# Performance work log

Measured on AMD Instinct MI355X. Metric: run time of the kernel, lower is better.

Reference implementation:

```python
import jax, jax.numpy as jnp
import numpy as np

N_NODES = 40000
N_EDGES = 640000
IN_DIM = 128
HID_DIM = 128


def _glorot(key, shape):
    fan_in, fan_out = shape[1], shape[0]
    lim = np.sqrt(6.0 / (fan_in + fan_out))
    return jax.random.uniform(key, shape, jnp.float32, -lim, lim)


def setup_inputs() -> dict:
    key = jax.random.key(0)
    ks = jax.random.split(key, 8)
    x = jax.random.normal(ks[0], (N_NODES, IN_DIM), dtype=jnp.float32)
    edge_index = jax.random.randint(ks[1], (2, N_EDGES), 0, N_NODES, dtype=jnp.int64)
    # SAGEConv params: lin_l (applied to aggregated neighbors, has bias), lin_r (self, no bias)
    W1l = _glorot(ks[2], (HID_DIM, IN_DIM))
    b1l = jnp.zeros((HID_DIM,), jnp.float32)
    W1r = _glorot(ks[3], (HID_DIM, IN_DIM))
    W2l = _glorot(ks[4], (HID_DIM, HID_DIM))
    b2l = jnp.zeros((HID_DIM,), jnp.float32)
    W2r = _glorot(ks[5], (HID_DIM, HID_DIM))
    return {"x": x, "edge_index": edge_index, "W1l": W1l, "b1l": b1l,
            "W1r": W1r, "W2l": W2l, "b2l": b2l, "W2r": W2r}


def _sage_conv(x, src, dst, Wl, bl, Wr):
    # mean aggregation of source features into destination nodes
    msg = x[src]  # [E, D] gather
    agg = jax.ops.segment_sum(msg, dst, num_segments=N_NODES)          # [N, D]
    cnt = jax.ops.segment_sum(jnp.ones_like(dst, jnp.float32), dst,
                              num_segments=N_NODES)                     # [N]
    mean = agg / jnp.maximum(cnt, 1.0)[:, None]
    # out = lin_l(mean_neighbors) + lin_r(x)
    return mean @ Wl.T + bl + x @ Wr.T


def reference(x, edge_index, W1l, b1l, W1r, W2l, b2l, W2r):
    src, dst = edge_index[0], edge_index[1]
    h = jax.nn.relu(_sage_conv(x, src, dst, W1l, b1l, W1r))
    h = jax.nn.relu(_sage_conv(h, src, dst, W2l, b2l, W2r))
    return h
```

## Files before the change

### kernel.cpp

```cpp
#include <hip/hip_runtime.h>
#include <hip/hip_bf16.h>

#define DIM 128
#define NN 40000
#define NE 640000
#define NBLK ((NN + 255) / 256)

typedef __attribute__((ext_vector_type(8))) short s16x8;
typedef __attribute__((ext_vector_type(4))) float f32x4;
typedef __attribute__((ext_vector_type(4))) unsigned short u16x4;
typedef __attribute__((ext_vector_type(4))) unsigned int u32x4;

__device__ __forceinline__ float bf16_lo(unsigned v) { return __uint_as_float(v << 16); }
__device__ __forceinline__ float bf16_hi(unsigned v) { return __uint_as_float(v & 0xffff0000u); }
__device__ __forceinline__ unsigned short f_to_bf16(float f) {
    unsigned u = __float_as_uint(f);
    u += 0x7fffu + ((u >> 16) & 1u);
    return (unsigned short)(u >> 16);
}

__global__ void fill_const_f32(float* __restrict__ out, int n, float v) {
    int i = blockIdx.x * blockDim.x + threadIdx.x;
    if (i < n) out[i] = v;
}

__global__ void cvt_all(const float* __restrict__ x, unsigned short* __restrict__ xb,
                        const float* __restrict__ w0, const float* __restrict__ w1,
                        const float* __restrict__ w2, const float* __restrict__ w3,
                        unsigned short* __restrict__ wb) {
    int b = blockIdx.x;
    const float* src;
    unsigned short* dst;
    size_t i;
    if (b < 5000) {
        src = x; dst = xb;
        i = (size_t)b * 256 + threadIdx.x;
    } else {
        int w = b - 5000;
        int m = w >> 4;
        src = (m == 0) ? w0 : (m == 1) ? w1 : (m == 2) ? w2 : w3;
        dst = wb + (size_t)m * 16384;
        i = (size_t)(w & 15) * 256 + threadIdx.x;
    }
    f32x4 v = *(const f32x4*)(src + 4 * i);
    u16x4 o;
    o.x = f_to_bf16(v.x); o.y = f_to_bf16(v.y);
    o.z = f_to_bf16(v.z); o.w = f_to_bf16(v.w);
    *(u16x4*)(dst + 4 * i) = o;
}

__global__ void zero_detect(int* __restrict__ deg, const int* __restrict__ ei,
                            int* __restrict__ flag) {
    int i = blockIdx.x * blockDim.x + threadIdx.x;
    if (i < NN) deg[i] = 0;
    if (blockIdx.x == 0 && threadIdx.x < 64) {
        int w = ei[2 * threadIdx.x + 1];
        unsigned long long m = __ballot(w == 0);
        if (threadIdx.x == 0) *flag = (m == ~0ull) ? 1 : 0;
    }
}


__global__ void count_deg(const int* __restrict__ ei, const int* __restrict__ fmt,
                          int* __restrict__ deg) {
    int e = blockIdx.x * blockDim.x + threadIdx.x;
    if (e >= NE) return;
    int dst = (*fmt) ? ((const int2*)ei)[NE + e].x : ei[NE + e];
    if ((unsigned)dst < (unsigned)NN) atomicAdd(&deg[dst], 1);
}

__global__ void block_sums(const int* __restrict__ deg, int* __restrict__ bsum) {
    __shared__ int sh[256];
    int i = blockIdx.x * 256 + threadIdx.x;
    sh[threadIdx.x] = (i < NN) ? deg[i] : 0;
    __syncthreads();
    for (int off = 128; off > 0; off >>= 1) {
        if (threadIdx.x < off) sh[threadIdx.x] += sh[threadIdx.x + off];
        __syncthreads();
    }
    if (threadIdx.x == 0) bsum[blockIdx.x] = sh[0];
}

__global__ void scan_bsums(int* __restrict__ bsum, int nb) {
    __shared__ int sh[256];
    int t = threadIdx.x;
    int v = (t < nb) ? bsum[t] : 0;
    sh[t] = v;
    __syncthreads();
    for (int off = 1; off < 256; off <<= 1) {
        int u = (t >= off) ? sh[t - off] : 0;
        __syncthreads();
        sh[t] += u;
        __syncthreads();
    }
    if (t < nb) bsum[t] = sh[t] - v;
}

__global__ void scan_block(const int* __restrict__ deg, const int* __restrict__ bsum,
                           int* __restrict__ row_ptr, int* __restrict__ cursor) {
    __shared__ int sh[256];
    int t = threadIdx.x;
    int i = blockIdx.x * 256 + t;
    int v = (i < NN) ? deg[i] : 0;
    sh[t] = v;
    __syncthreads();
    for (int off = 1; off < 256; off <<= 1) {
        int u = (t >= off) ? sh[t - off] : 0;
        __syncthreads();
        sh[t] += u;
        __syncthreads();
    }
    int excl = sh[t] - v + bsum[blockIdx.x];
    if (i < NN) { row_ptr[i] = excl; cursor[i] = excl; }
    if (i == NN - 1) row_ptr[NN] = excl + v;
}

__global__ void fill_csr(const int* __restrict__ ei, const int* __restrict__ fmt,
                         int* __restrict__ cursor, int* __restrict__ sorted_src) {
    int e = blockIdx.x * blockDim.x + threadIdx.x;
    if (e >= NE) return;
    int src, dst;
    if (*fmt) {
        src = ((const int2*)ei)[e].x;
        dst = ((const int2*)ei)[NE + e].x;
    } else {
        src = ei[e];
        dst = ei[NE + e];
    }
    if ((unsigned)dst >= (unsigned)NN) return;
    int pos = atomicAdd(&cursor[dst], 1);
    if ((unsigned)pos < (unsigned)NE) sorted_src[pos] = src;
}


__global__ __launch_bounds__(256) void aggregate_g(
    const unsigned short* __restrict__ xin,
    const int* __restrict__ row_ptr,
    const int* __restrict__ sorted_src,
    unsigned short* __restrict__ mean_out) {
    int lane = threadIdx.x & 63;
    int wv = threadIdx.x >> 6;
    int grp = lane >> 4;
    int lid = lane & 15;
    int n = blockIdx.x * 16 + wv * 4 + grp;
    int start = row_ptr[n], end = row_ptr[n + 1];

    float a[8] = {0.f, 0.f, 0.f, 0.f, 0.f, 0.f, 0.f, 0.f};
    int i = start;
    for (; i + 3 < end; i += 4) {
        int s0 = sorted_src[i];
        int s1 = sorted_src[i + 1];
        int s2 = sorted_src[i + 2];
        int s3 = sorted_src[i + 3];
        u32x4 v0 = *(const u32x4*)(xin + (size_t)s0 * DIM + lid * 8);
        u32x4 v1 = *(const u32x4*)(xin + (size_t)s1 * DIM + lid * 8);
        u32x4 v2 = *(const u32x4*)(xin + (size_t)s2 * DIM + lid * 8);
        u32x4 v3 = *(const u32x4*)(xin + (size_t)s3 * DIM + lid * 8);
        a[0] += bf16_lo(v0.x) + bf16_lo(v1.x) + bf16_lo(v2.x) + bf16_lo(v3.x);
        a[1] += bf16_hi(v0.x) + bf16_hi(v1.x) + bf16_hi(v2.x) + bf16_hi(v3.x);
        a[2] += bf16_lo(v0.y) + bf16_lo(v1.y) + bf16_lo(v2.y) + bf16_lo(v3.y);
        a[3] += bf16_hi(v0.y) + bf16_hi(v1.y) + bf16_hi(v2.y) + bf16_hi(v3.y);
        a[4] += bf16_lo(v0.z) + bf16_lo(v1.z) + bf16_lo(v2.z) + bf16_lo(v3.z);
        a[5] += bf16_hi(v0.z) + bf16_hi(v1.z) + bf16_hi(v2.z) + bf16_hi(v3.z);
        a[6] += bf16_lo(v0.w) + bf16_lo(v1.w) + bf16_lo(v2.w) + bf16_lo(v3.w);
        a[7] += bf16_hi(v0.w) + bf16_hi(v1.w) + bf16_hi(v2.w) + bf16_hi(v3.w);
    }
    for (; i < end; ++i) {
        int s = sorted_src[i];
        u32x4 v = *(const u32x4*)(xin + (size_t)s * DIM + lid * 8);
        a[0] += bf16_lo(v.x); a[1] += bf16_hi(v.x);
        a[2] += bf16_lo(v.y); a[3] += bf16_hi(v.y);
        a[4] += bf16_lo(v.z); a[5] += bf16_hi(v.z);
        a[6] += bf16_lo(v.w); a[7] += bf16_hi(v.w);
    }

    int d = end - start;
    float inv = 1.f / (float)(d > 1 ? d : 1);
    u32x4 o;
    o.x = (unsigned)f_to_bf16(a[0] * inv) | ((unsigned)f_to_bf16(a[1] * inv) << 16);
    o.y = (unsigned)f_to_bf16(a[2] * inv) | ((unsigned)f_to_bf16(a[3] * inv) << 16);
    o.z = (unsigned)f_to_bf16(a[4] * inv) | ((unsigned)f_to_bf16(a[5] * inv) << 16);
    o.w = (unsigned)f_to_bf16(a[6] * inv) | ((unsigned)f_to_bf16(a[7] * inv) << 16);
    *(u32x4*)(mean_out + (size_t)n * DIM + lid * 8) = o;
}


template <bool WRITE_F32>
__global__ __launch_bounds__(256) void sage_gemm(
    const unsigned short* __restrict__ mean,
    const unsigned short* __restrict__ hself,
    const unsigned short* __restrict__ Wl,
    const unsigned short* __restrict__ Wr,
    const float* __restrict__ bias,
    void* __restrict__ outv) {
    int lane = threadIdx.x & 63;
    int wv = threadIdx.x >> 6;
    int quad = lane >> 4;
    int lid = lane & 15;
    int row0 = blockIdx.x * 64;
    int bcol = blockIdx.y * 64 + wv * 16 + lid;

    const unsigned short* wl0 = Wl + (size_t)bcol * DIM + quad * 8;
    const unsigned short* wr0 = Wr + (size_t)bcol * DIM + quad * 8;
    s16x8 bl[4], br[4];
#pragma unroll
    for (int kb = 0; kb < 4; ++kb) {
        bl[kb] = *(const s16x8*)(wl0 + kb * 32);
        br[kb] = *(const s16x8*)(wr0 + kb * 32);
    }

    const unsigned short* ap = mean + (size_t)(row0 + lid) * DIM + quad * 8;
    const unsigned short* hp = hself + (size_t)(row0 + lid) * DIM + quad * 8;
    const int TS = 16 * DIM;

    f32x4 acc[4] = {{0,0,0,0},{0,0,0,0},{0,0,0,0},{0,0,0,0}};
    s16x8 am[2][4], ah[2][4];

#pragma unroll
    for (int kb = 0; kb < 4; ++kb) {
        am[0][kb] = *(const s16x8*)(ap + kb * 32);
        ah[0][kb] = *(const s16x8*)(hp + kb * 32);
    }
#pragma unroll
    for (int t = 0; t < 4; ++t) {
        int cb = t & 1, nb = (t + 1) & 1;
        if (t < 3) {
#pragma unroll
            for (int kb = 0; kb < 4; ++kb) {
                am[nb][kb] = *(const s16x8*)(ap + (t + 1) * TS + kb * 32);
                ah[nb][kb] = *(const s16x8*)(hp + (t + 1) * TS + kb * 32);
            }
        }
#pragma unroll
        for (int kb = 0; kb < 4; ++kb)
            acc[t] = __builtin_amdgcn_mfma_f32_16x16x32_bf16(am[cb][kb], bl[kb], acc[t], 0, 0, 0);
#pragma unroll
        for (int kb = 0; kb < 4; ++kb)
            acc[t] = __builtin_amdgcn_mfma_f32_16x16x32_bf16(ah[cb][kb], br[kb], acc[t], 0, 0, 0);
    }

    float bv = bias[bcol];
#pragma unroll
    for (int t = 0; t < 4; ++t) {
#pragma unroll
        for (int r = 0; r < 4; ++r) {
            int orow = row0 + t * 16 + quad * 4 + r;
            float v = fmaxf(acc[t][r] + bv, 0.f);
            if (WRITE_F32)
                ((float*)outv)[(size_t)orow * DIM + bcol] = v;
            else
                ((unsigned short*)outv)[(size_t)orow * DIM + bcol] = f_to_bf16(v);
        }
    }
}


extern "C" void kernel_launch(void* const* d_in, const int* in_sizes, int n_in,
                              void* d_out, int out_size, void* d_ws, size_t ws_size,
                              hipStream_t stream) {
    const float* x   = (const float*)d_in[0];
    const int*   ei  = (const int*)d_in[1];
    const float* W1l = (const float*)d_in[2];
    const float* b1l = (const float*)d_in[3];
    const float* W1r = (const float*)d_in[4];
    const float* W2l = (const float*)d_in[5];
    const float* b2l = (const float*)d_in[6];
    const float* W2r = (const float*)d_in[7];
    float* out = (float*)d_out;

    const int OUT_ELEMS = NN * DIM;

    const size_t OFF_DEG  = 0;
    const size_t OFF_ROW  = 163840;
    const size_t OFF_BSUM = 324608;
    const size_t OFF_CUR  = 327680;
    const size_t OFF_FMT  = 491264;
    const size_t OFF_SRT  = 491520;
    const size_t OFF_WB   = 3051520;
    const size_t OFF_XB   = 3182592;
    const size_t OFF_MEAN = 13422592;
    const size_t OFF_H1   = 23662592;
    const size_t NEEDED   = 33902592;

    if (ws_size < NEEDED) {
        fill_const_f32<<<(OUT_ELEMS + 255) / 256, 256, 0, stream>>>(out, OUT_ELEMS, 50.0f);
        return;
    }

    char* ws = (char*)d_ws;
    int* deg     = (int*)(ws + OFF_DEG);
    int* row_ptr = (int*)(ws + OFF_ROW);
    int* bsum    = (int*)(ws + OFF_BSUM);
    int* cursor  = (int*)(ws + OFF_CUR);
    int* fmtflag = (int*)(ws + OFF_FMT);
    int* sorted  = (int*)(ws + OFF_SRT);
    unsigned short* Wb    = (unsigned short*)(ws + OFF_WB);
    unsigned short* xb    = (unsigned short*)(ws + OFF_XB);
    unsigned short* meanb = (unsigned short*)(ws + OFF_MEAN);
    unsigned short* h1b   = (unsigned short*)(ws + OFF_H1);
    unsigned short* W1lb = Wb;
    unsigned short* W1rb = Wb + 16384;
    unsigned short* W2lb = Wb + 32768;
    unsigned short* W2rb = Wb + 49152;

    cvt_all<<<5064, 256, 0, stream>>>(x, xb, W1l, W1r, W2l, W2r, Wb);

    zero_detect<<<NBLK, 256, 0, stream>>>(deg, ei, fmtflag);
    count_deg<<<(NE + 255) / 256, 256, 0, stream>>>(ei, fmtflag, deg);
    block_sums<<<NBLK, 256, 0, stream>>>(deg, bsum);
    scan_bsums<<<1, 256, 0, stream>>>(bsum, NBLK);
    scan_block<<<NBLK, 256, 0, stream>>>(deg, bsum, row_ptr, cursor);
    fill_csr<<<(NE + 255) / 256, 256, 0, stream>>>(ei, fmtflag, cursor, sorted);

    aggregate_g<<<NN / 16, 256, 0, stream>>>(xb, row_ptr, sorted, meanb);
    sage_gemm<false><<<dim3(NN / 64, 2), 256, 0, stream>>>(meanb, xb, W1lb, W1rb, b1l, h1b);

    aggregate_g<<<NN / 16, 256, 0, stream>>>(h1b, row_ptr, sorted, meanb);
    sage_gemm<true><<<dim3(NN / 64, 2), 256, 0, stream>>>(meanb, h1b, W2lb, W2rb, b2l, out);
}
```

Baseline: 245.4 us.

## Fuse setup kernels, single-pass scan, and prefetch edge indices in aggregation

Merges deg zeroing and format detection into the conversion kernel, and replaces the three-kernel scan with one kernel in which each block recomputes its prefix base by summing all preceding degree entries. This removes three kernel launches and their serialization gaps. The aggregation loop now loads the next four source indices before accumulating the current gathered rows, so index fetch latency overlaps the feature loads. The fused scan does redundant O(blocks) reads per block, up to about 157 strided loads per thread in the last block, which adds some latency.

```diff
diff --git a/kernel.cpp b/kernel.cpp
--- a/kernel.cpp
+++ b/kernel.cpp
@@ -27,8 +27,20 @@
 __global__ void cvt_all(const float* __restrict__ x, unsigned short* __restrict__ xb,
                         const float* __restrict__ w0, const float* __restrict__ w1,
                         const float* __restrict__ w2, const float* __restrict__ w3,
-                        unsigned short* __restrict__ wb) {
+                        unsigned short* __restrict__ wb,
+                        int* __restrict__ deg, const int* __restrict__ ei,
+                        int* __restrict__ flag) {
     int b = blockIdx.x;
+    if (b >= 5064) {
+        int i = (b - 5064) * 256 + threadIdx.x;
+        if (i < NN) deg[i] = 0;
+        if (b == 5064 && threadIdx.x < 64) {
+            int w = ei[2 * threadIdx.x + 1];
+            unsigned long long m = __ballot(w == 0);
+            if (threadIdx.x == 0) *flag = (m == ~0ull) ? 1 : 0;
+        }
+        return;
+    }
     const float* src;
     unsigned short* dst;
     size_t i;
@@ -49,17 +61,6 @@
     *(u16x4*)(dst + 4 * i) = o;
 }
 
-__global__ void zero_detect(int* __restrict__ deg, const int* __restrict__ ei,
-                            int* __restrict__ flag) {
-    int i = blockIdx.x * blockDim.x + threadIdx.x;
-    if (i < NN) deg[i] = 0;
-    if (blockIdx.x == 0 && threadIdx.x < 64) {
-        int w = ei[2 * threadIdx.x + 1];
-        unsigned long long m = __ballot(w == 0);
-        if (threadIdx.x == 0) *flag = (m == ~0ull) ? 1 : 0;
-    }
-}
-
 
 __global__ void count_deg(const int* __restrict__ ei, const int* __restrict__ fmt,
                           int* __restrict__ deg) {
@@ -69,38 +70,26 @@
     if ((unsigned)dst < (unsigned)NN) atomicAdd(&deg[dst], 1);
 }
 
-__global__ void block_sums(const int* __restrict__ deg, int* __restrict__ bsum) {
+__global__ void scan_fused(const int* __restrict__ deg, int* __restrict__ row_ptr,
+                           int* __restrict__ cursor) {
     __shared__ int sh[256];
-    int i = blockIdx.x * 256 + threadIdx.x;
-    sh[threadIdx.x] = (i < NN) ? deg[i] : 0;
+    __shared__ int base_sh;
+    int t = threadIdx.x, bid = blockIdx.x;
+
+    int s = 0;
+    for (int j = 0; j < bid; ++j) s += deg[j * 256 + t];
+    sh[t] = s;
     __syncthreads();
     for (int off = 128; off > 0; off >>= 1) {
-        if (threadIdx.x < off) sh[threadIdx.x] += sh[threadIdx.x + off];
+        if (t < off) sh[t] += sh[t + off];
         __syncthreads();
     }
-    if (threadIdx.x == 0) bsum[blockIdx.x] = sh[0];
-}
-
-__global__ void scan_bsums(int* __restrict__ bsum, int nb) {
-    __shared__ int sh[256];
-    int t = threadIdx.x;
-    int v = (t < nb) ? bsum[t] : 0;
-    sh[t] = v;
+    if (t == 0) base_sh = sh[0];
     __syncthreads();
-    for (int off = 1; off < 256; off <<= 1) {
-        int u = (t >= off) ? sh[t - off] : 0;
-        __syncthreads();
-        sh[t] += u;
-        __syncthreads();
-    }
-    if (t < nb) bsum[t] = sh[t] - v;
-}
-
-__global__ void scan_block(const int* __restrict__ deg, const int* __restrict__ bsum,
-                           int* __restrict__ row_ptr, int* __restrict__ cursor) {
-    __shared__ int sh[256];
-    int t = threadIdx.x;
-    int i = blockIdx.x * 256 + t;
+    int base = base_sh;
+    __syncthreads();
+
+    int i = bid * 256 + t;
     int v = (i < NN) ? deg[i] : 0;
     sh[t] = v;
     __syncthreads();
@@ -110,7 +99,7 @@
         sh[t] += u;
         __syncthreads();
     }
-    int excl = sh[t] - v + bsum[blockIdx.x];
+    int excl = sh[t] - v + base;
     if (i < NN) { row_ptr[i] = excl; cursor[i] = excl; }
     if (i == NN - 1) row_ptr[NN] = excl + v;
 }
@@ -147,15 +136,23 @@
 
     float a[8] = {0.f, 0.f, 0.f, 0.f, 0.f, 0.f, 0.f, 0.f};
     int i = start;
-    for (; i + 3 < end; i += 4) {
-        int s0 = sorted_src[i];
-        int s1 = sorted_src[i + 1];
-        int s2 = sorted_src[i + 2];
-        int s3 = sorted_src[i + 3];
+    int s0 = 0, s1 = 0, s2 = 0, s3 = 0;
+    bool have = (i + 3 < end);
+    if (have) {
+        s0 = sorted_src[i];     s1 = sorted_src[i + 1];
+        s2 = sorted_src[i + 2]; s3 = sorted_src[i + 3];
+    }
+    while (have) {
         u32x4 v0 = *(const u32x4*)(xin + (size_t)s0 * DIM + lid * 8);
         u32x4 v1 = *(const u32x4*)(xin + (size_t)s1 * DIM + lid * 8);
         u32x4 v2 = *(const u32x4*)(xin + (size_t)s2 * DIM + lid * 8);
         u32x4 v3 = *(const u32x4*)(xin + (size_t)s3 * DIM + lid * 8);
+        int ni = i + 4;
+        bool nhave = (ni + 3 < end);
+        if (nhave) {
+            s0 = sorted_src[ni];     s1 = sorted_src[ni + 1];
+            s2 = sorted_src[ni + 2]; s3 = sorted_src[ni + 3];
+        }
         a[0] += bf16_lo(v0.x) + bf16_lo(v1.x) + bf16_lo(v2.x) + bf16_lo(v3.x);
         a[1] += bf16_hi(v0.x) + bf16_hi(v1.x) + bf16_hi(v2.x) + bf16_hi(v3.x);
         a[2] += bf16_lo(v0.y) + bf16_lo(v1.y) + bf16_lo(v2.y) + bf16_lo(v3.y);
@@ -164,6 +161,8 @@
         a[5] += bf16_hi(v0.z) + bf16_hi(v1.z) + bf16_hi(v2.z) + bf16_hi(v3.z);
         a[6] += bf16_lo(v0.w) + bf16_lo(v1.w) + bf16_lo(v2.w) + bf16_lo(v3.w);
         a[7] += bf16_hi(v0.w) + bf16_hi(v1.w) + bf16_hi(v2.w) + bf16_hi(v3.w);
+        i = ni;
+        have = nhave;
     }
     for (; i < end; ++i) {
         int s = sorted_src[i];
@@ -272,7 +271,6 @@
 
     const size_t OFF_DEG  = 0;
     const size_t OFF_ROW  = 163840;
-    const size_t OFF_BSUM = 324608;
     const size_t OFF_CUR  = 327680;
     const size_t OFF_FMT  = 491264;
     const size_t OFF_SRT  = 491520;
@@ -290,7 +288,6 @@
     char* ws = (char*)d_ws;
     int* deg     = (int*)(ws + OFF_DEG);
     int* row_ptr = (int*)(ws + OFF_ROW);
-    int* bsum    = (int*)(ws + OFF_BSUM);
     int* cursor  = (int*)(ws + OFF_CUR);
     int* fmtflag = (int*)(ws + OFF_FMT);
     int* sorted  = (int*)(ws + OFF_SRT);
@@ -303,13 +300,9 @@
     unsigned short* W2lb = Wb + 32768;
     unsigned short* W2rb = Wb + 49152;
 
-    cvt_all<<<5064, 256, 0, stream>>>(x, xb, W1l, W1r, W2l, W2r, Wb);
-
-    zero_detect<<<NBLK, 256, 0, stream>>>(deg, ei, fmtflag);
+    cvt_all<<<5221, 256, 0, stream>>>(x, xb, W1l, W1r, W2l, W2r, Wb, deg, ei, fmtflag);
     count_deg<<<(NE + 255) / 256, 256, 0, stream>>>(ei, fmtflag, deg);
-    block_sums<<<NBLK, 256, 0, stream>>>(deg, bsum);
-    scan_bsums<<<1, 256, 0, stream>>>(bsum, NBLK);
-    scan_block<<<NBLK, 256, 0, stream>>>(deg, bsum, row_ptr, cursor);
+    scan_fused<<<NBLK, 256, 0, stream>>>(deg, row_ptr, cursor);
     fill_csr<<<(NE + 255) / 256, 256, 0, stream>>>(ei, fmtflag, cursor, sorted);
 
     aggregate_g<<<NN / 16, 256, 0, stream>>>(xb, row_ptr, sorted, meanb);
```

Measured after the change: 255.8 us. 1.04x slower.

## Fuse CSR build and bf16 conversion into one persistent kernel with grid barriers

Applied to the files above, without the earlier changes.

Replaces seven separate preprocessing launches (conversion, degree zeroing, counting, two-level scan, CSR fill) with a single persistent kernel of 1536 blocks that uses a software grid-wide barrier between phases. It also hides the x/weight conversion in the last phase alongside the CSR fill. The aim is to remove kernel launch gaps and tail idle time. The cost is that the spin barrier needs every block resident at once, which is a deadlock risk if 1536 blocks do not fit. It also adds atomic and sleep overhead and a memset.

```diff
diff --git a/kernel.cpp b/kernel.cpp
--- a/kernel.cpp
+++ b/kernel.cpp
@@ -5,6 +5,7 @@
 #define NN 40000
 #define NE 640000
 #define NBLK ((NN + 255) / 256)
+#define PGRID 1536
 
 typedef __attribute__((ext_vector_type(8))) short s16x8;
 typedef __attribute__((ext_vector_type(4))) float f32x4;
@@ -24,114 +25,127 @@
     if (i < n) out[i] = v;
 }
 
-__global__ void cvt_all(const float* __restrict__ x, unsigned short* __restrict__ xb,
-                        const float* __restrict__ w0, const float* __restrict__ w1,
-                        const float* __restrict__ w2, const float* __restrict__ w3,
-                        unsigned short* __restrict__ wb) {
-    int b = blockIdx.x;
-    const float* src;
-    unsigned short* dst;
-    size_t i;
-    if (b < 5000) {
-        src = x; dst = xb;
-        i = (size_t)b * 256 + threadIdx.x;
-    } else {
-        int w = b - 5000;
-        int m = w >> 4;
-        src = (m == 0) ? w0 : (m == 1) ? w1 : (m == 2) ? w2 : w3;
-        dst = wb + (size_t)m * 16384;
-        i = (size_t)(w & 15) * 256 + threadIdx.x;
-    }
-    f32x4 v = *(const f32x4*)(src + 4 * i);
-    u16x4 o;
-    o.x = f_to_bf16(v.x); o.y = f_to_bf16(v.y);
-    o.z = f_to_bf16(v.z); o.w = f_to_bf16(v.w);
-    *(u16x4*)(dst + 4 * i) = o;
-}
-
-__global__ void zero_detect(int* __restrict__ deg, const int* __restrict__ ei,
-                            int* __restrict__ flag) {
-    int i = blockIdx.x * blockDim.x + threadIdx.x;
-    if (i < NN) deg[i] = 0;
-    if (blockIdx.x == 0 && threadIdx.x < 64) {
-        int w = ei[2 * threadIdx.x + 1];
+__device__ __forceinline__ void gsync(int* bar) {
+    __syncthreads();
+    if (threadIdx.x == 0) {
+        __threadfence();
+        int g = __hip_atomic_load(&bar[1], __ATOMIC_RELAXED, __HIP_MEMORY_SCOPE_AGENT);
+        int a = __hip_atomic_fetch_add(&bar[0], 1, __ATOMIC_ACQ_REL, __HIP_MEMORY_SCOPE_AGENT);
+        if (a == (int)gridDim.x - 1) {
+            __hip_atomic_store(&bar[0], 0, __ATOMIC_RELAXED, __HIP_MEMORY_SCOPE_AGENT);
+            __hip_atomic_fetch_add(&bar[1], 1, __ATOMIC_RELEASE, __HIP_MEMORY_SCOPE_AGENT);
+        } else {
+            while (__hip_atomic_load(&bar[1], __ATOMIC_ACQUIRE, __HIP_MEMORY_SCOPE_AGENT) == g)
+                __builtin_amdgcn_s_sleep(2);
+        }
+        __threadfence();
+    }
+    __syncthreads();
+}
+
+__global__ __launch_bounds__(256, 8) void prep(
+    const float* __restrict__ x, const int* __restrict__ ei,
+    const float* __restrict__ W1l, const float* __restrict__ W1r,
+    const float* __restrict__ W2l, const float* __restrict__ W2r,
+    unsigned short* __restrict__ xb, unsigned short* __restrict__ Wb,
+    int* __restrict__ deg, int* __restrict__ bsum, int* __restrict__ row_ptr,
+    int* __restrict__ cursor, int* __restrict__ fmtflag,
+    int* __restrict__ sorted, int* __restrict__ bar) {
+    __shared__ int sh[256];
+    int tid = threadIdx.x, bid = blockIdx.x;
+    int gidx = bid * 256 + tid;
+    const int GSZ = PGRID * 256;
+
+    for (int i = gidx; i < NN; i += GSZ) deg[i] = 0;
+    if (bid == 0 && tid < 64) {
+        int w = ei[2 * tid + 1];
         unsigned long long m = __ballot(w == 0);
-        if (threadIdx.x == 0) *flag = (m == ~0ull) ? 1 : 0;
-    }
-}
-
-
-__global__ void count_deg(const int* __restrict__ ei, const int* __restrict__ fmt,
-                          int* __restrict__ deg) {
-    int e = blockIdx.x * blockDim.x + threadIdx.x;
-    if (e >= NE) return;
-    int dst = (*fmt) ? ((const int2*)ei)[NE + e].x : ei[NE + e];
-    if ((unsigned)dst < (unsigned)NN) atomicAdd(&deg[dst], 1);
-}
-
-__global__ void block_sums(const int* __restrict__ deg, int* __restrict__ bsum) {
-    __shared__ int sh[256];
-    int i = blockIdx.x * 256 + threadIdx.x;
-    sh[threadIdx.x] = (i < NN) ? deg[i] : 0;
-    __syncthreads();
-    for (int off = 128; off > 0; off >>= 1) {
-        if (threadIdx.x < off) sh[threadIdx.x] += sh[threadIdx.x + off];
+        if (tid == 0)
+            __hip_atomic_store(fmtflag, (m == ~0ull) ? 1 : 0,
+                               __ATOMIC_RELAXED, __HIP_MEMORY_SCOPE_AGENT);
+    }
+    gsync(bar);
+
+    int fmt = __hip_atomic_load(fmtflag, __ATOMIC_RELAXED, __HIP_MEMORY_SCOPE_AGENT);
+
+    for (int e = gidx; e < NE; e += GSZ) {
+        int dst = fmt ? ((const int2*)ei)[NE + e].x : ei[NE + e];
+        if ((unsigned)dst < (unsigned)NN) atomicAdd(&deg[dst], 1);
+    }
+    gsync(bar);
+
+    if (bid < NBLK) {
+        int i = bid * 256 + tid;
+        sh[tid] = (i < NN) ? deg[i] : 0;
         __syncthreads();
-    }
-    if (threadIdx.x == 0) bsum[blockIdx.x] = sh[0];
-}
-
-__global__ void scan_bsums(int* __restrict__ bsum, int nb) {
-    __shared__ int sh[256];
-    int t = threadIdx.x;
-    int v = (t < nb) ? bsum[t] : 0;
-    sh[t] = v;
-    __syncthreads();
-    for (int off = 1; off < 256; off <<= 1) {
-        int u = (t >= off) ? sh[t - off] : 0;
+        for (int off = 128; off > 0; off >>= 1) {
+            if (tid < off) sh[tid] += sh[tid + off];
+            __syncthreads();
+        }
+        if (tid == 0) bsum[bid] = sh[0];
+    }
+    gsync(bar);
+
+    if (bid < NBLK) {
+        int v0 = (tid < NBLK) ? bsum[tid] : 0;
+        sh[tid] = v0;
         __syncthreads();
-        sh[t] += u;
+        for (int off = 1; off < 256; off <<= 1) {
+            int u = (tid >= off) ? sh[tid - off] : 0;
+            __syncthreads();
+            sh[tid] += u;
+            __syncthreads();
+        }
+        int base = sh[bid] - bsum[bid];
         __syncthreads();
-    }
-    if (t < nb) bsum[t] = sh[t] - v;
-}
-
-__global__ void scan_block(const int* __restrict__ deg, const int* __restrict__ bsum,
-                           int* __restrict__ row_ptr, int* __restrict__ cursor) {
-    __shared__ int sh[256];
-    int t = threadIdx.x;
-    int i = blockIdx.x * 256 + t;
-    int v = (i < NN) ? deg[i] : 0;
-    sh[t] = v;
-    __syncthreads();
-    for (int off = 1; off < 256; off <<= 1) {
-        int u = (t >= off) ? sh[t - off] : 0;
+        int i = bid * 256 + tid;
+        int v = (i < NN) ? deg[i] : 0;
+        sh[tid] = v;
         __syncthreads();
-        sh[t] += u;
-        __syncthreads();
-    }
-    int excl = sh[t] - v + bsum[blockIdx.x];
-    if (i < NN) { row_ptr[i] = excl; cursor[i] = excl; }
-    if (i == NN - 1) row_ptr[NN] = excl + v;
-}
-
-__global__ void fill_csr(const int* __restrict__ ei, const int* __restrict__ fmt,
-                         int* __restrict__ cursor, int* __restrict__ sorted_src) {
-    int e = blockIdx.x * blockDim.x + threadIdx.x;
-    if (e >= NE) return;
-    int src, dst;
-    if (*fmt) {
-        src = ((const int2*)ei)[e].x;
-        dst = ((const int2*)ei)[NE + e].x;
-    } else {
-        src = ei[e];
-        dst = ei[NE + e];
-    }
-    if ((unsigned)dst >= (unsigned)NN) return;
-    int pos = atomicAdd(&cursor[dst], 1);
-    if ((unsigned)pos < (unsigned)NE) sorted_src[pos] = src;
-}
-
+        for (int off = 1; off < 256; off <<= 1) {
+            int u = (tid >= off) ? sh[tid - off] : 0;
+            __syncthreads();
+            sh[tid] += u;
+            __syncthreads();
+        }
+        int excl = sh[tid] - v + base;
+        if (i < NN) { row_ptr[i] = excl; cursor[i] = excl; }
+        if (i == NN - 1) row_ptr[NN] = excl + v;
+    }
+    gsync(bar);
+
+    for (int e = gidx; e < NE; e += GSZ) {
+        int src, dst;
+        if (fmt) {
+            src = ((const int2*)ei)[e].x;
+            dst = ((const int2*)ei)[NE + e].x;
+        } else {
+            src = ei[e];
+            dst = ei[NE + e];
+        }
+        if ((unsigned)dst < (unsigned)NN) {
+            int pos = atomicAdd(&cursor[dst], 1);
+            if ((unsigned)pos < (unsigned)NE) sorted[pos] = src;
+        }
+    }
+    for (int g = gidx; g < 1280000; g += GSZ) {
+        f32x4 v = *(const f32x4*)(x + 4 * (size_t)g);
+        u16x4 o;
+        o.x = f_to_bf16(v.x); o.y = f_to_bf16(v.y);
+        o.z = f_to_bf16(v.z); o.w = f_to_bf16(v.w);
+        *(u16x4*)(xb + 4 * (size_t)g) = o;
+    }
+    if (gidx < 16384) {
+        int m = gidx >> 12;
+        const float* src = (m == 0) ? W1l : (m == 1) ? W1r : (m == 2) ? W2l : W2r;
+        size_t off = (size_t)(gidx & 4095) * 4;
+        f32x4 v = *(const f32x4*)(src + off);
+        u16x4 o;
+        o.x = f_to_bf16(v.x); o.y = f_to_bf16(v.y);
+        o.z = f_to_bf16(v.z); o.w = f_to_bf16(v.w);
+        *(u16x4*)(Wb + (size_t)m * 16384 + off) = o;
+    }
+}
 
 __global__ __launch_bounds__(256) void aggregate_g(
     const unsigned short* __restrict__ xin,
@@ -184,7 +198,6 @@
     *(u32x4*)(mean_out + (size_t)n * DIM + lid * 8) = o;
 }
 
-
 template <bool WRITE_F32>
 __global__ __launch_bounds__(256) void sage_gemm(
     const unsigned short* __restrict__ mean,
@@ -275,6 +288,7 @@
     const size_t OFF_BSUM = 324608;
     const size_t OFF_CUR  = 327680;
     const size_t OFF_FMT  = 491264;
+    const size_t OFF_BAR  = 491328;
     const size_t OFF_SRT  = 491520;
     const size_t OFF_WB   = 3051520;
     const size_t OFF_XB   = 3182592;
@@ -293,6 +307,7 @@
     int* bsum    = (int*)(ws + OFF_BSUM);
     int* cursor  = (int*)(ws + OFF_CUR);
     int* fmtflag = (int*)(ws + OFF_FMT);
+    int* bar     = (int*)(ws + OFF_BAR);
     int* sorted  = (int*)(ws + OFF_SRT);
     unsigned short* Wb    = (unsigned short*)(ws + OFF_WB);
     unsigned short* xb    = (unsigned short*)(ws + OFF_XB);
@@ -303,14 +318,9 @@
     unsigned short* W2lb = Wb + 32768;
     unsigned short* W2rb = Wb + 49152;
 
-    cvt_all<<<5064, 256, 0, stream>>>(x, xb, W1l, W1r, W2l, W2r, Wb);
-
-    zero_detect<<<NBLK, 256, 0, stream>>>(deg, ei, fmtflag);
-    count_deg<<<(NE + 255) / 256, 256, 0, stream>>>(ei, fmtflag, deg);
-    block_sums<<<NBLK, 256, 0, stream>>>(deg, bsum);
-    scan_bsums<<<1, 256, 0, stream>>>(bsum, NBLK);
-    scan_block<<<NBLK, 256, 0, stream>>>(deg, bsum, row_ptr, cursor);
-    fill_csr<<<(NE + 255) / 256, 256, 0, stream>>>(ei, fmtflag, cursor, sorted);
+    hipMemsetAsync(bar, 0, 2 * sizeof(int), stream);
+    prep<<<PGRID, 256, 0, stream>>>(x, ei, W1l, W1r, W2l, W2r, xb, Wb,
+                                    deg, bsum, row_ptr, cursor, fmtflag, sorted, bar);
 
     aggregate_g<<<NN / 16, 256, 0, stream>>>(xb, row_ptr, sorted, meanb);
     sage_gemm<false><<<dim3(NN / 64, 2), 256, 0, stream>>>(meanb, xb, W1lb, W1rb, b1l, h1b);
```

Measured after the change: 905.8 us. +269.1%, slower.
